# Optimization experiments

Measured on AMD Instinct MI355X. Metric: run time of the kernel, lower is better.

The kernel has to match this reference:

```python
import jax, jax.numpy as jnp
import numpy as np

C_EM, H_EM, C_A = 256, 8, 32
S, R = 1024, 256
LN_EPS = 1e-5
MASK_BIAS = 1e9


def setup_inputs() -> dict:
    key = jax.random.key(0)
    ks = jax.random.split(key, 8)
    sc = 0.02
    m = jax.random.normal(ks[0], (S, R, C_EM), jnp.float32)
    # binary column mask (float mask in the original; int here so it is a constant)
    mask = (jax.random.uniform(ks[1], (S, R)) < 0.9).astype(jnp.int32)
    return {
        "m": m,
        "ln_g": jnp.ones((C_EM,), jnp.float32),
        "ln_b": jnp.zeros((C_EM,), jnp.float32),
        "w_q": jax.random.normal(ks[2], (C_EM, H_EM, C_A), jnp.float32) * sc,
        "w_k": jax.random.normal(ks[3], (C_EM, C_A), jnp.float32) * sc,
        "w_v": jax.random.normal(ks[4], (C_EM, C_A), jnp.float32) * sc,
        "w_g": jax.random.normal(ks[5], (C_EM, H_EM, C_A), jnp.float32) * sc,
        "b_g": jnp.zeros((H_EM, C_A), jnp.float32),
        "w_o": jax.random.normal(ks[6], (H_EM, C_A, C_EM), jnp.float32) * sc,
        "b_o": jnp.zeros((C_EM,), jnp.float32),
        "mask": mask,
    }


def reference(m, ln_g, ln_b, w_q, w_k, w_v, w_g, b_g, w_o, b_o, mask):
    maskf = mask.astype(m.dtype)  # [s, r]
    # LayerNorm over c_em (biased variance, eps=1e-5, torch default)
    mu = jnp.mean(m, axis=-1, keepdims=True)
    var = jnp.mean((m - mu) ** 2, axis=-1, keepdims=True)
    x = (m - mu) * jax.lax.rsqrt(var + LN_EPS) * ln_g + ln_b  # [s, r, c]
    # masked mean-pool over s -> per-column query
    q_pool = jnp.sum(x * maskf[..., None], axis=-3) / (jnp.sum(maskf, axis=-2)[..., None] + 1e-10)  # [r, c]
    Q = jnp.einsum('rc,chd->rhd', q_pool, w_q) * (1.0 / np.sqrt(C_A))  # [r, h, d]
    K = jnp.einsum('src,cd->srd', x, w_k)  # [s, r, d]
    V = jnp.einsum('src,cd->srd', x, w_v)  # [s, r, d]
    G = jax.nn.sigmoid(jnp.einsum('src,chd->srhd', x, w_g) + b_g)  # [s, r, h, d]
    bias = (maskf - 1.0) * MASK_BIAS  # [s, r]
    logits = jnp.einsum('rhd,srd->srh', Q, K) + bias[..., None]  # [s, r, h]
    A = jax.nn.softmax(logits, axis=-3)  # softmax over s
    O = jnp.einsum('srh,srd->rhd', A, V)  # [r, h, d]
    out = jnp.einsum('srhd,hdc->src', O[None, :, :, :] * G, w_o) + b_o  # [s, r, c]
    return out
```

## Files before the change

### kernel.cpp

```cpp
#include <hip/hip_runtime.h>
#include <math.h>

#define S_DIM 1024
#define R_DIM 256
#define C_DIM 256
#define SCALE 0.17677669529663687f

typedef short bf16x8 __attribute__((ext_vector_type(8)));
typedef float f32x4 __attribute__((ext_vector_type(4)));

__device__ __forceinline__ float wred(float v) {
#pragma unroll
  for (int m = 32; m >= 1; m >>= 1) v += __shfl_xor(v, m, 64);
  return v;
}

__device__ __forceinline__ short f2bf(float f) {
  union { float f; unsigned u; } v;
  v.f = f;
  unsigned r = v.u + 0x7fffu + ((v.u >> 16) & 1u);
  return (short)(r >> 16);
}

__device__ __forceinline__ float bf2f(short s) {
  union { unsigned u; float f; } v;
  v.u = ((unsigned)(unsigned short)s) << 16;
  return v.f;
}

__global__ __launch_bounds__(256)
void k0_prep(const float* __restrict__ w_g, const float* __restrict__ w_o,
             const float* __restrict__ w_k, const float* __restrict__ w_v,
             short* __restrict__ wgB, short* __restrict__ woB,
             short* __restrict__ wkvB) {
  const int id = blockIdx.x * 256 + threadIdx.x;
  if (id < 16384) {
    const int which = id >> 13;
    const int s = id & 8191;
    const int n = s & 255, g = (s >> 8) & 3, kb = s >> 10;
    const float* W = which ? w_o : w_g;
    short* Out = which ? woB : wgB;
#pragma unroll
    for (int j = 0; j < 8; ++j)
      Out[(((size_t)kb * 256 + n) * 4 + g) * 8 + j] =
          f2bf(W[(size_t)(kb * 32 + g * 8 + j) * 256 + n]);
  } else {
    const int s = id - 16384;
    const int n = s & 63, g = (s >> 6) & 3, kb = s >> 8;
    const float* W = (n < 32) ? w_k : w_v;
    const int nn = n & 31;
#pragma unroll
    for (int j = 0; j < 8; ++j)
      wkvB[(((size_t)kb * 64 + n) * 4 + g) * 8 + j] =
          f2bf(W[(size_t)(kb * 32 + g * 8 + j) * 32 + nn]);
  }
}

__global__ __launch_bounds__(256, 3)
void k1_ln_kv(const float* __restrict__ mIn, const float* __restrict__ ln_g,
              const float* __restrict__ ln_b, const short* __restrict__ wkvB,
              const int* __restrict__ mask,
              float* __restrict__ mu_ws, float* __restrict__ rs_ws,
              float* __restrict__ K_ws, float* __restrict__ V_ws,
              float* __restrict__ pool_ws) {
  __shared__ __align__(16) short A_lds[2048 * 8];
  __shared__ float mask_s[64];
  __shared__ float4 poolp[4][64];
  const int r  = blockIdx.y;
  const int s0 = blockIdx.x * 64;
  const int t  = threadIdx.x;

  if (t < 64) mask_s[t] = mask[(s0 + t) * R_DIM + r] ? 1.f : 0.f;

  {
    const int rw = t >> 2;
    const int q  = t & 3;
    const size_t p = (size_t)(s0 + rw) * R_DIM + r;
    const float* src = mIn + p * C_DIM + q * 64;
    float4 xv[16];
    float sum = 0.f, ssq = 0.f;
#pragma unroll
    for (int i = 0; i < 16; ++i) {
      xv[i] = *(const float4*)(src + i * 4);
      sum += xv[i].x + xv[i].y + xv[i].z + xv[i].w;
      ssq += xv[i].x * xv[i].x + xv[i].y * xv[i].y + xv[i].z * xv[i].z +
             xv[i].w * xv[i].w;
    }
    sum += __shfl_xor(sum, 1, 64); ssq += __shfl_xor(ssq, 1, 64);
    sum += __shfl_xor(sum, 2, 64); ssq += __shfl_xor(ssq, 2, 64);
    const float mu = sum * (1.f / 256.f);
    const float var = ssq * (1.f / 256.f) - mu * mu;
    const float rs = rsqrtf(var + 1e-5f);
    if (q == 0) { mu_ws[p] = mu; rs_ws[p] = rs; }

    const int gw = rw >> 4;
    const int lf0 = rw & 15;
#pragma unroll
    for (int kh = 0; kh < 2; ++kh) {
      const int kb = 2 * q + kh;
#pragma unroll
      for (int g = 0; g < 4; ++g) {
        const int lidx = kh * 32 + g * 8;
        const float4 a0 = xv[lidx >> 2], a1 = xv[(lidx >> 2) + 1];
        const float4 g0 = *(const float4*)(ln_g + kb * 32 + g * 8);
        const float4 g1 = *(const float4*)(ln_g + kb * 32 + g * 8 + 4);
        const float4 b0 = *(const float4*)(ln_b + kb * 32 + g * 8);
        const float4 b1 = *(const float4*)(ln_b + kb * 32 + g * 8 + 4);
        bf16x8 f;
        f[0] = f2bf((a0.x - mu) * rs * g0.x + b0.x);
        f[1] = f2bf((a0.y - mu) * rs * g0.y + b0.y);
        f[2] = f2bf((a0.z - mu) * rs * g0.z + b0.z);
        f[3] = f2bf((a0.w - mu) * rs * g0.w + b0.w);
        f[4] = f2bf((a1.x - mu) * rs * g1.x + b1.x);
        f[5] = f2bf((a1.y - mu) * rs * g1.y + b1.y);
        f[6] = f2bf((a1.z - mu) * rs * g1.z + b1.z);
        f[7] = f2bf((a1.w - mu) * rs * g1.w + b1.w);
        int byte = (((gw * 8 + kb) * 64 + lf0 + g * 16) << 4) ^ (((kb >> 1) & 3) << 5);
        *(bf16x8*)((char*)A_lds + byte) = f;
      }
    }
  }
  __syncthreads();

  {
    const int w = t >> 6, l = t & 63;
    const int lm = l & 15, g = l >> 4;
    f32x4 acc[4];
#pragma unroll
    for (int ni = 0; ni < 4; ++ni) acc[ni] = (f32x4){0.f, 0.f, 0.f, 0.f};
#pragma unroll
    for (int kb = 0; kb < 8; ++kb) {
      const int byte = (((w * 8 + kb) * 64 + l) << 4) ^ (((kb >> 1) & 3) << 5);
      const bf16x8 a = *(const bf16x8*)((char*)A_lds + byte);
      bf16x8 bfr[4];
#pragma unroll
      for (int ni = 0; ni < 4; ++ni)
        bfr[ni] = *(const bf16x8*)(wkvB + (((size_t)kb * 64 + lm + ni * 16) * 4 + g) * 8);
#pragma unroll
      for (int ni = 0; ni < 4; ++ni)
        acc[ni] = __builtin_amdgcn_mfma_f32_16x16x32_bf16(a, bfr[ni], acc[ni], 0, 0, 0);
    }
#pragma unroll
    for (int ni = 0; ni < 4; ++ni) {
      const int col = lm + ni * 16;
      float* Out = (col < 32) ? K_ws : V_ws;
      const int cc = col & 31;
#pragma unroll
      for (int reg = 0; reg < 4; ++reg) {
        const int s = s0 + w * 16 + g * 4 + reg;
        Out[((size_t)s * R_DIM + r) * 32 + cc] = acc[ni][reg];
      }
    }
  }

  {
    const int lc = t & 63;
    const int wq = t >> 6;
    const int kb = lc >> 3, g2 = (lc >> 1) & 3, bh = (lc & 1) * 4;
    float4 ps = make_float4(0.f, 0.f, 0.f, 0.f);
    for (int i = 0; i < 16; ++i) {
      const int rloc = (i + lc) & 15;
      const int byte =
          ((((wq * 8 + kb) * 64 + rloc + g2 * 16) << 4) + bh * 2) ^ (((kb >> 1) & 3) << 5);
      const short4 xb = *(const short4*)((char*)A_lds + byte);
      const float mk = mask_s[wq * 16 + rloc];
      ps.x += mk * bf2f(xb.x);
      ps.y += mk * bf2f(xb.y);
      ps.z += mk * bf2f(xb.z);
      ps.w += mk * bf2f(xb.w);
    }
    poolp[wq][lc] = ps;
  }
  __syncthreads();
  if (t < 64) {
    const float4 a = poolp[0][t], b = poolp[1][t], c = poolp[2][t], d = poolp[3][t];
    atomicAdd(&pool_ws[r * C_DIM + t * 4 + 0], a.x + b.x + c.x + d.x);
    atomicAdd(&pool_ws[r * C_DIM + t * 4 + 1], a.y + b.y + c.y + d.y);
    atomicAdd(&pool_ws[r * C_DIM + t * 4 + 2], a.z + b.z + c.z + d.z);
    atomicAdd(&pool_ws[r * C_DIM + t * 4 + 3], a.w + b.w + c.w + d.w);
  }
}

__global__ __launch_bounds__(256, 2)
void k2_q(const float* __restrict__ pool_ws, const int* __restrict__ mask,
          const float* __restrict__ w_q, float* __restrict__ Q_ws) {
  __shared__ float qp[256];
  __shared__ float wsum[4];
  const int r = blockIdx.x, t = threadIdx.x;
  int cnt = 0;
  for (int s = t; s < S_DIM; s += 256) cnt += mask[s * R_DIM + r];
  float cf = wred((float)cnt);
  if ((t & 63) == 0) wsum[t >> 6] = cf;
  __syncthreads();
  const float denom = wsum[0] + wsum[1] + wsum[2] + wsum[3] + 1e-10f;
  qp[t] = pool_ws[r * C_DIM + t] / denom;
  __syncthreads();
  float acc = 0.f;
  for (int c = 0; c < 256; ++c) acc += qp[c] * w_q[c * 256 + t];
  Q_ws[r * 256 + t] = acc * SCALE;
}

__global__ __launch_bounds__(256, 2)
void k3_attn(const float* __restrict__ K_ws, const float* __restrict__ V_ws,
             const int* __restrict__ mask, const float* __restrict__ Q_ws,
             float* __restrict__ O_ws) {
  __shared__ float q[256];
  __shared__ float lg[1024 * 9];
  __shared__ float kv[256 * 36];
  __shared__ float mh[8], inv[8];
  const int r = blockIdx.x, t = threadIdx.x;
  q[t] = Q_ws[r * 256 + t];

  for (int ch = 0; ch < 4; ++ch) {
    const int sb = ch * 256;
    __syncthreads();
    for (int f = t; f < 2048; f += 256) {
      const int sl = f >> 3, dq = f & 7;
      *(float4*)(kv + sl * 36 + dq * 4) =
          *(const float4*)(K_ws + ((size_t)(sb + sl) * R_DIM + r) * 32 + dq * 4);
    }
    __syncthreads();
    float kr[32];
#pragma unroll
    for (int dq = 0; dq < 8; ++dq)
      *(float4*)(kr + dq * 4) = *(float4*)(kv + t * 36 + dq * 4);
    const float bias = mask[(sb + t) * R_DIM + r] ? 0.f : -1e9f;
#pragma unroll
    for (int h = 0; h < 8; ++h) {
      float a = 0.f;
#pragma unroll
      for (int d = 0; d < 32; ++d) a += q[h * 32 + d] * kr[d];
      lg[(sb + t) * 9 + h] = a + bias;
    }
  }
  __syncthreads();
  {
    const int h = t >> 5, l32 = t & 31;
    float mx = -INFINITY;
    for (int k = 0; k < 32; ++k) mx = fmaxf(mx, lg[(l32 + 32 * k) * 9 + h]);
#pragma unroll
    for (int mk = 16; mk >= 1; mk >>= 1) mx = fmaxf(mx, __shfl_xor(mx, mk, 64));
    float sm = 0.f;
    for (int k = 0; k < 32; ++k) sm += expf(lg[(l32 + 32 * k) * 9 + h] - mx);
#pragma unroll
    for (int mk = 16; mk >= 1; mk >>= 1) sm += __shfl_xor(sm, mk, 64);
    if (l32 == 0) { mh[h] = mx; inv[h] = 1.f / sm; }
  }
  __syncthreads();
  for (int f = t; f < 8192; f += 256) {
    const int s = f >> 3, h = f & 7;
    lg[s * 9 + h] = expf(lg[s * 9 + h] - mh[h]) * inv[h];
  }
  const int h = t >> 5, d = t & 31;
  float o = 0.f;
  for (int ch = 0; ch < 4; ++ch) {
    const int sb = ch * 256;
    __syncthreads();
    for (int f = t; f < 2048; f += 256) {
      const int sl = f >> 3, dq = f & 7;
      *(float4*)(kv + sl * 36 + dq * 4) =
          *(const float4*)(V_ws + ((size_t)(sb + sl) * R_DIM + r) * 32 + dq * 4);
    }
    __syncthreads();
    for (int sl = 0; sl < 256; ++sl)
      o += lg[(sb + sl) * 9 + h] * kv[sl * 36 + d];
  }
  O_ws[r * 256 + t] = o;
}

__global__ __launch_bounds__(256, 2)
void k4_mfma(const float* __restrict__ mIn, const float* __restrict__ ln_g,
             const float* __restrict__ ln_b, const float* __restrict__ mu_ws,
             const float* __restrict__ rs_ws, const short* __restrict__ wgB,
             const float* __restrict__ b_g, const float* __restrict__ O_ws,
             const short* __restrict__ woB, const float* __restrict__ b_o,
             float* __restrict__ out) {
  __shared__ __align__(16) short A_lds[2048 * 8];
  const int t = threadIdx.x;
  const int p0 = blockIdx.x * 64;
  const int r0 = p0 & 255;
  const int l = t & 63;
  const int w = t >> 6;
  const int lm = l & 15;
  const int g = l >> 4;

  {
    const int row = w * 16 + lm;
    const size_t p = (size_t)(p0 + row);
    const float mu = mu_ws[p], rs = rs_ws[p];
    const float* mrow = mIn + p * 256 + g * 8;
    const float* gp = ln_g + g * 8;
    const float* bp = ln_b + g * 8;
#pragma unroll
    for (int kb = 0; kb < 8; ++kb) {
      const float4 m0 = *(const float4*)(mrow + kb * 32);
      const float4 m1 = *(const float4*)(mrow + kb * 32 + 4);
      const float4 g0 = *(const float4*)(gp + kb * 32);
      const float4 g1 = *(const float4*)(gp + kb * 32 + 4);
      const float4 b0 = *(const float4*)(bp + kb * 32);
      const float4 b1 = *(const float4*)(bp + kb * 32 + 4);
      bf16x8 xf;
      xf[0] = f2bf((m0.x - mu) * rs * g0.x + b0.x);
      xf[1] = f2bf((m0.y - mu) * rs * g0.y + b0.y);
      xf[2] = f2bf((m0.z - mu) * rs * g0.z + b0.z);
      xf[3] = f2bf((m0.w - mu) * rs * g0.w + b0.w);
      xf[4] = f2bf((m1.x - mu) * rs * g1.x + b1.x);
      xf[5] = f2bf((m1.y - mu) * rs * g1.y + b1.y);
      xf[6] = f2bf((m1.z - mu) * rs * g1.z + b1.z);
      xf[7] = f2bf((m1.w - mu) * rs * g1.w + b1.w);
      *(bf16x8*)(A_lds + ((w * 8 + kb) * 64 + l) * 8) = xf;
    }
  }
  __syncthreads();

  const int nB = w * 64;
  const int col = nB + lm;
  f32x4 acc[4][4];

#pragma unroll
  for (int ni = 0; ni < 4; ++ni) {
    const float bg = b_g[col + ni * 16];
#pragma unroll
    for (int mi = 0; mi < 4; ++mi) acc[mi][ni] = (f32x4){bg, bg, bg, bg};
  }
#pragma unroll
  for (int kb = 0; kb < 8; ++kb) {
    bf16x8 a[4], bb[4];
#pragma unroll
    for (int mi = 0; mi < 4; ++mi)
      a[mi] = *(const bf16x8*)(A_lds + ((mi * 8 + kb) * 64 + l) * 8);
#pragma unroll
    for (int ni = 0; ni < 4; ++ni)
      bb[ni] = *(const bf16x8*)(wgB + (((size_t)kb * 256 + col + ni * 16) * 4 + g) * 8);
#pragma unroll
    for (int mi = 0; mi < 4; ++mi)
#pragma unroll
      for (int ni = 0; ni < 4; ++ni)
        acc[mi][ni] = __builtin_amdgcn_mfma_f32_16x16x32_bf16(a[mi], bb[ni], acc[mi][ni], 0, 0, 0);
  }
  __syncthreads();

#pragma unroll
  for (int mi = 0; mi < 4; ++mi) {
#pragma unroll
    for (int ni = 0; ni < 4; ++ni) {
      const int c2 = col + ni * 16;
      const int kb2 = c2 >> 5, g2 = (c2 >> 3) & 3, b2 = c2 & 7;
#pragma unroll
      for (int reg = 0; reg < 4; ++reg) {
        const int row = mi * 16 + g * 4 + reg;
        const float o = O_ws[(r0 + row) * 256 + c2];
        const float gl = acc[mi][ni][reg];
        const float tv = o / (1.f + expf(-gl));
        A_lds[((mi * 8 + kb2) * 64 + (g * 4 + reg) + g2 * 16) * 8 + b2] = f2bf(tv);
      }
    }
  }
  __syncthreads();

#pragma unroll
  for (int ni = 0; ni < 4; ++ni) {
    const float bo = b_o[col + ni * 16];
#pragma unroll
    for (int mi = 0; mi < 4; ++mi) acc[mi][ni] = (f32x4){bo, bo, bo, bo};
  }
#pragma unroll
  for (int kb = 0; kb < 8; ++kb) {
    bf16x8 a[4], bb[4];
#pragma unroll
    for (int mi = 0; mi < 4; ++mi)
      a[mi] = *(const bf16x8*)(A_lds + ((mi * 8 + kb) * 64 + l) * 8);
#pragma unroll
    for (int ni = 0; ni < 4; ++ni)
      bb[ni] = *(const bf16x8*)(woB + (((size_t)kb * 256 + col + ni * 16) * 4 + g) * 8);
#pragma unroll
    for (int mi = 0; mi < 4; ++mi)
#pragma unroll
      for (int ni = 0; ni < 4; ++ni)
        acc[mi][ni] = __builtin_amdgcn_mfma_f32_16x16x32_bf16(a[mi], bb[ni], acc[mi][ni], 0, 0, 0);
  }

#pragma unroll
  for (int mi = 0; mi < 4; ++mi)
#pragma unroll
    for (int ni = 0; ni < 4; ++ni)
#pragma unroll
      for (int reg = 0; reg < 4; ++reg) {
        const int row = mi * 16 + g * 4 + reg;
        out[(size_t)(p0 + row) * 256 + col + ni * 16] = acc[mi][ni][reg];
      }
}

extern "C" void kernel_launch(void* const* d_in, const int* in_sizes, int n_in,
                              void* d_out, int out_size, void* d_ws, size_t ws_size,
                              hipStream_t stream) {
  const float* mIn  = (const float*)d_in[0];
  const float* ln_g = (const float*)d_in[1];
  const float* ln_b = (const float*)d_in[2];
  const float* w_q  = (const float*)d_in[3];
  const float* w_k  = (const float*)d_in[4];
  const float* w_v  = (const float*)d_in[5];
  const float* w_g  = (const float*)d_in[6];
  const float* b_g  = (const float*)d_in[7];
  const float* w_o  = (const float*)d_in[8];
  const float* b_o  = (const float*)d_in[9];
  const int*   mask = (const int*)d_in[10];
  float* outp = (float*)d_out;

  char* ws = (char*)d_ws;
  const size_t NP = (size_t)S_DIM * R_DIM;
  float* mu_ws   = (float*)ws;
  float* rs_ws   = mu_ws + NP;
  float* K_ws    = rs_ws + NP;
  float* V_ws    = K_ws + NP * 32;
  float* pool_ws = V_ws + NP * 32;
  float* Q_ws    = pool_ws + 65536;
  float* O_ws    = Q_ws + 65536;
  short* wgB     = (short*)(O_ws + 65536);
  short* woB     = wgB + 65536;
  short* wkvB    = woB + 65536;

  hipMemsetAsync(pool_ws, 0, 65536 * sizeof(float), stream);

  k0_prep<<<72, 256, 0, stream>>>(w_g, w_o, w_k, w_v, wgB, woB, wkvB);
  k1_ln_kv<<<dim3(S_DIM / 64, R_DIM), 256, 0, stream>>>(
      mIn, ln_g, ln_b, wkvB, mask, mu_ws, rs_ws, K_ws, V_ws, pool_ws);
  k2_q<<<R_DIM, 256, 0, stream>>>(pool_ws, mask, w_q, Q_ws);
  k3_attn<<<R_DIM, 256, 0, stream>>>(K_ws, V_ws, mask, Q_ws, O_ws);
  k4_mfma<<<S_DIM * R_DIM / 64, 256, 0, stream>>>(
      mIn, ln_g, ln_b, mu_ws, rs_ws, wgB, b_g, O_ws, woB, b_o, outp);
}
```

Before: 376.6 us.

## Stash normalized bf16 activations in output buffer to skip recomputing LayerNorm

k1 now writes the LayerNorm'd bf16 tile (512 bytes per row) into the output buffer, using it as scratch, and drops the mu/rs workspace. k4 reads those bf16 rows back instead of re-reading the fp32 input and renormalizing, which halves its activation read traffic. k4 also switches to an (s-block, r) grid so O is loaded once per block, uses __expf, and raises occupancy to 3. Each block overwrites its own rows in place, which relies on every row being fully read before it is written and on per-row ownership being unchanged between k1 and k4.

Result: slower. 398.0 us (+5.7%).

```diff
diff --git a/kernel.cpp b/kernel.cpp
--- a/kernel.cpp
+++ b/kernel.cpp
@@ -60,9 +60,8 @@
 void k1_ln_kv(const float* __restrict__ mIn, const float* __restrict__ ln_g,
               const float* __restrict__ ln_b, const short* __restrict__ wkvB,
               const int* __restrict__ mask,
-              float* __restrict__ mu_ws, float* __restrict__ rs_ws,
               float* __restrict__ K_ws, float* __restrict__ V_ws,
-              float* __restrict__ pool_ws) {
+              float* __restrict__ pool_ws, char* xout) {
   __shared__ __align__(16) short A_lds[2048 * 8];
   __shared__ float mask_s[64];
   __shared__ float4 poolp[4][64];
@@ -91,7 +90,6 @@
     const float mu = sum * (1.f / 256.f);
     const float var = ssq * (1.f / 256.f) - mu * mu;
     const float rs = rsqrtf(var + 1e-5f);
-    if (q == 0) { mu_ws[p] = mu; rs_ws[p] = rs; }
 
     const int gw = rw >> 4;
     const int lf0 = rw & 15;
@@ -123,6 +121,16 @@
   __syncthreads();
 
   {
+#pragma unroll
+    for (int i = 0; i < 8; ++i) {
+      const int u = i * 256 + t;
+      const bf16x8 v = *(const bf16x8*)((const char*)A_lds + u * 16);
+      *(bf16x8*)(xout + ((size_t)((s0 + (u >> 5)) * R_DIM + r)) * 1024 +
+                 (u & 31) * 16) = v;
+    }
+  }
+
+  {
     const int w = t >> 6, l = t & 63;
     const int lm = l & 15, g = l >> 4;
     f32x4 acc[4];
@@ -268,67 +276,43 @@
   O_ws[r * 256 + t] = o;
 }
 
-__global__ __launch_bounds__(256, 2)
-void k4_mfma(const float* __restrict__ mIn, const float* __restrict__ ln_g,
-             const float* __restrict__ ln_b, const float* __restrict__ mu_ws,
-             const float* __restrict__ rs_ws, const short* __restrict__ wgB,
-             const float* __restrict__ b_g, const float* __restrict__ O_ws,
-             const short* __restrict__ woB, const float* __restrict__ b_o,
-             float* __restrict__ out) {
-  __shared__ __align__(16) short A_lds[2048 * 8];
+__global__ __launch_bounds__(256, 3)
+void k4_mfma(const short* __restrict__ wgB, const float* __restrict__ b_g,
+             const float* __restrict__ O_ws, const short* __restrict__ woB,
+             const float* __restrict__ b_o, float* outx) {
+  __shared__ __align__(16) short T_lds[2048 * 8];
   const int t = threadIdx.x;
-  const int p0 = blockIdx.x * 64;
-  const int r0 = p0 & 255;
-  const int l = t & 63;
-  const int w = t >> 6;
-  const int lm = l & 15;
-  const int g = l >> 4;
-
-  {
-    const int row = w * 16 + lm;
-    const size_t p = (size_t)(p0 + row);
-    const float mu = mu_ws[p], rs = rs_ws[p];
-    const float* mrow = mIn + p * 256 + g * 8;
-    const float* gp = ln_g + g * 8;
-    const float* bp = ln_b + g * 8;
-#pragma unroll
-    for (int kb = 0; kb < 8; ++kb) {
-      const float4 m0 = *(const float4*)(mrow + kb * 32);
-      const float4 m1 = *(const float4*)(mrow + kb * 32 + 4);
-      const float4 g0 = *(const float4*)(gp + kb * 32);
-      const float4 g1 = *(const float4*)(gp + kb * 32 + 4);
-      const float4 b0 = *(const float4*)(bp + kb * 32);
-      const float4 b1 = *(const float4*)(bp + kb * 32 + 4);
-      bf16x8 xf;
-      xf[0] = f2bf((m0.x - mu) * rs * g0.x + b0.x);
-      xf[1] = f2bf((m0.y - mu) * rs * g0.y + b0.y);
-      xf[2] = f2bf((m0.z - mu) * rs * g0.z + b0.z);
-      xf[3] = f2bf((m0.w - mu) * rs * g0.w + b0.w);
-      xf[4] = f2bf((m1.x - mu) * rs * g1.x + b1.x);
-      xf[5] = f2bf((m1.y - mu) * rs * g1.y + b1.y);
-      xf[6] = f2bf((m1.z - mu) * rs * g1.z + b1.z);
-      xf[7] = f2bf((m1.w - mu) * rs * g1.w + b1.w);
-      *(bf16x8*)(A_lds + ((w * 8 + kb) * 64 + l) * 8) = xf;
-    }
-  }
-  __syncthreads();
-
-  const int nB = w * 64;
-  const int col = nB + lm;
+  const int s0 = blockIdx.x * 64;
+  const int r  = blockIdx.y;
+  const int l = t & 63, w = t >> 6, lm = l & 15, g = l >> 4;
+  const char* outB = (const char*)outx;
+  const int col = w * 64 + lm;
+
+  float o4[4], bg4[4], bo4[4];
+#pragma unroll
+  for (int ni = 0; ni < 4; ++ni) {
+    o4[ni] = O_ws[r * 256 + col + ni * 16];
+    bg4[ni] = b_g[col + ni * 16];
+    bo4[ni] = b_o[col + ni * 16];
+  }
+
   f32x4 acc[4][4];
-
-#pragma unroll
-  for (int ni = 0; ni < 4; ++ni) {
-    const float bg = b_g[col + ni * 16];
-#pragma unroll
-    for (int mi = 0; mi < 4; ++mi) acc[mi][ni] = (f32x4){bg, bg, bg, bg};
-  }
+#pragma unroll
+  for (int ni = 0; ni < 4; ++ni)
+#pragma unroll
+    for (int mi = 0; mi < 4; ++mi)
+      acc[mi][ni] = (f32x4){bg4[ni], bg4[ni], bg4[ni], bg4[ni]};
+
 #pragma unroll
   for (int kb = 0; kb < 8; ++kb) {
+    const int cc = ((kb >> 1) & 3) << 1;
     bf16x8 a[4], bb[4];
 #pragma unroll
-    for (int mi = 0; mi < 4; ++mi)
-      a[mi] = *(const bf16x8*)(A_lds + ((mi * 8 + kb) * 64 + l) * 8);
+    for (int mi = 0; mi < 4; ++mi) {
+      const int u = ((mi * 8 + kb) * 64 + l) ^ cc;
+      a[mi] = *(const bf16x8*)(outB +
+              ((size_t)((s0 + (u >> 5)) * R_DIM + r)) * 1024 + (u & 31) * 16);
+    }
 #pragma unroll
     for (int ni = 0; ni < 4; ++ni)
       bb[ni] = *(const bf16x8*)(wgB + (((size_t)kb * 256 + col + ni * 16) * 4 + g) * 8);
@@ -338,38 +322,32 @@
       for (int ni = 0; ni < 4; ++ni)
         acc[mi][ni] = __builtin_amdgcn_mfma_f32_16x16x32_bf16(a[mi], bb[ni], acc[mi][ni], 0, 0, 0);
   }
-  __syncthreads();
-
-#pragma unroll
-  for (int mi = 0; mi < 4; ++mi) {
+
+#pragma unroll
+  for (int mi = 0; mi < 4; ++mi)
 #pragma unroll
     for (int ni = 0; ni < 4; ++ni) {
       const int c2 = col + ni * 16;
       const int kb2 = c2 >> 5, g2 = (c2 >> 3) & 3, b2 = c2 & 7;
 #pragma unroll
       for (int reg = 0; reg < 4; ++reg) {
-        const int row = mi * 16 + g * 4 + reg;
-        const float o = O_ws[(r0 + row) * 256 + c2];
-        const float gl = acc[mi][ni][reg];
-        const float tv = o / (1.f + expf(-gl));
-        A_lds[((mi * 8 + kb2) * 64 + (g * 4 + reg) + g2 * 16) * 8 + b2] = f2bf(tv);
+        const float tv = o4[ni] / (1.f + __expf(-acc[mi][ni][reg]));
+        T_lds[((mi * 8 + kb2) * 64 + (g * 4 + reg) + g2 * 16) * 8 + b2] = f2bf(tv);
       }
     }
-  }
-  __syncthreads();
-
-#pragma unroll
-  for (int ni = 0; ni < 4; ++ni) {
-    const float bo = b_o[col + ni * 16];
-#pragma unroll
-    for (int mi = 0; mi < 4; ++mi) acc[mi][ni] = (f32x4){bo, bo, bo, bo};
-  }
+  __syncthreads();
+
+#pragma unroll
+  for (int ni = 0; ni < 4; ++ni)
+#pragma unroll
+    for (int mi = 0; mi < 4; ++mi)
+      acc[mi][ni] = (f32x4){bo4[ni], bo4[ni], bo4[ni], bo4[ni]};
 #pragma unroll
   for (int kb = 0; kb < 8; ++kb) {
     bf16x8 a[4], bb[4];
 #pragma unroll
     for (int mi = 0; mi < 4; ++mi)
-      a[mi] = *(const bf16x8*)(A_lds + ((mi * 8 + kb) * 64 + l) * 8);
+      a[mi] = *(const bf16x8*)(T_lds + ((mi * 8 + kb) * 64 + l) * 8);
 #pragma unroll
     for (int ni = 0; ni < 4; ++ni)
       bb[ni] = *(const bf16x8*)(woB + (((size_t)kb * 256 + col + ni * 16) * 4 + g) * 8);
@@ -387,7 +365,8 @@
 #pragma unroll
       for (int reg = 0; reg < 4; ++reg) {
         const int row = mi * 16 + g * 4 + reg;
-        out[(size_t)(p0 + row) * 256 + col + ni * 16] = acc[mi][ni][reg];
+        outx[((size_t)((s0 + row) * R_DIM + r)) * 256 + col + ni * 16] =
+            acc[mi][ni][reg];
       }
 }
 
@@ -409,9 +388,7 @@
 
   char* ws = (char*)d_ws;
   const size_t NP = (size_t)S_DIM * R_DIM;
-  float* mu_ws   = (float*)ws;
-  float* rs_ws   = mu_ws + NP;
-  float* K_ws    = rs_ws + NP;
+  float* K_ws    = (float*)ws;
   float* V_ws    = K_ws + NP * 32;
   float* pool_ws = V_ws + NP * 32;
   float* Q_ws    = pool_ws + 65536;
@@ -424,9 +401,9 @@
 
   k0_prep<<<72, 256, 0, stream>>>(w_g, w_o, w_k, w_v, wgB, woB, wkvB);
   k1_ln_kv<<<dim3(S_DIM / 64, R_DIM), 256, 0, stream>>>(
-      mIn, ln_g, ln_b, wkvB, mask, mu_ws, rs_ws, K_ws, V_ws, pool_ws);
+      mIn, ln_g, ln_b, wkvB, mask, K_ws, V_ws, pool_ws, (char*)outp);
   k2_q<<<R_DIM, 256, 0, stream>>>(pool_ws, mask, w_q, Q_ws);
   k3_attn<<<R_DIM, 256, 0, stream>>>(K_ws, V_ws, mask, Q_ws, O_ws);
-  k4_mfma<<<S_DIM * R_DIM / 64, 256, 0, stream>>>(
-      mIn, ln_g, ln_b, mu_ws, rs_ws, wgB, b_g, O_ws, woB, b_o, outp);
-}
+  k4_mfma<<<dim3(S_DIM / 64, R_DIM), 256, 0, stream>>>(
+      wgB, b_g, O_ws, woB, b_o, outp);
+}
```
